# Optimization experiments

Measured on AMD Instinct MI355X. Metric: run time of the kernel, lower is better.

## Reference

```python
import jax, jax.numpy as jnp
import numpy as np

B, T, C, L = 512, 512, 96, 64   # batch, time steps, num classes (incl. blank), max label len
BLANK = C - 1                   # keras ctc_batch_cost uses last class as blank
EPS = 1e-7                      # epsilon added before log, as in ctc_batch_cost
NEG = -1e30                     # log-space -inf surrogate


def setup_inputs():
    key = jax.random.key(0)
    k1, k2, k3 = jax.random.split(key, 3)
    # y_pred is a softmax output: positive, rows sum to 1
    u = jax.random.uniform(k1, (B, T, C), dtype=jnp.float32, minval=0.1, maxval=1.0)
    y_pred = u / jnp.sum(u, axis=-1, keepdims=True)
    # labels in [0, BLANK), variable lengths, padded with -1 (as the layer expects)
    labels = jax.random.randint(k2, (B, L), 0, C - 1, dtype=jnp.int32)
    lens = jax.random.randint(k3, (B,), L // 2, L + 1, dtype=jnp.int32)
    y_true = jnp.where(jnp.arange(L)[None, :] < lens[:, None], labels, -1)
    return {"y_true": y_true, "y_pred": y_pred}


def _ctc_loss(y_true, y_pred):
    """Per-example CTC negative log-likelihood (forward DP in log space)."""
    y_true = y_true.astype(jnp.int32)
    lbl_len = jnp.sum((y_true != -1).astype(jnp.int32), axis=-1)          # (B,)
    labels = jnp.where(y_true != -1, y_true, 0)                            # (B,L)

    S = 2 * L + 1
    # extended label: blank, l0, blank, l1, ..., blank
    ext = jnp.full((B, S), BLANK, dtype=jnp.int32).at[:, 1::2].set(labels)  # (B,S)
    ext_m2 = jnp.pad(ext[:, :-2], ((0, 0), (2, 0)), constant_values=BLANK)
    can_skip = (ext != BLANK) & (ext != ext_m2)                             # (B,S)

    lp = jnp.log(y_pred.astype(jnp.float32) + EPS)   # (B,T,C) log-probs
    lp_t = jnp.swapaxes(lp, 0, 1)                    # (T,B,C) for scan over time

    emit0 = jnp.take_along_axis(lp_t[0], ext, axis=1)                       # (B,S)
    alpha0 = (jnp.full((B, S), NEG, dtype=jnp.float32)
              .at[:, 0].set(emit0[:, 0])
              .at[:, 1].set(emit0[:, 1]))

    def step(alpha, lpt):
        a1 = jnp.pad(alpha[:, :-1], ((0, 0), (1, 0)), constant_values=NEG)
        a2 = jnp.pad(alpha[:, :-2], ((0, 0), (2, 0)), constant_values=NEG)
        a2 = jnp.where(can_skip, a2, NEG)
        m = jnp.maximum(alpha, jnp.maximum(a1, a2))
        lse = m + jnp.log(jnp.exp(alpha - m) + jnp.exp(a1 - m) + jnp.exp(a2 - m))
        alpha_new = lse + jnp.take_along_axis(lpt, ext, axis=1)
        return alpha_new, None

    alphaT, _ = jax.lax.scan(step, alpha0, lp_t[1:])

    # total log-prob ends at last blank (s=2*len) or last label (s=2*len-1)
    i_blank = (2 * lbl_len)[:, None]
    i_label = jnp.maximum(2 * lbl_len - 1, 0)[:, None]
    a_b = jnp.take_along_axis(alphaT, i_blank, axis=1)[:, 0]
    a_l = jnp.take_along_axis(alphaT, i_label, axis=1)[:, 0]
    return -jnp.logaddexp(a_b, a_l)                                         # (B,)


def reference(y_true, y_pred):
    # layer adds tf.reduce_mean(ctc_batch_cost(...)) as the model loss
    return jnp.mean(_ctc_loss(y_true, y_pred))
```

## Files before the change

### kernel.cpp

```cpp
#include <hip/hip_runtime.h>


#define B_ 512
#define T_ 512
#define C_ 96
#define L_ 64
#define BLANK_ 95
#define EPSF 1e-7f
#define LN2F 0.69314718055994530942f

template <int CTRL>
__device__ __forceinline__ float dpp_mov(float x) {
    return __int_as_float(
        __builtin_amdgcn_update_dpp(0, __float_as_int(x), CTRL, 0xF, 0xF, true));
}

__device__ __forceinline__ float wave_max(float m) {
    m = fmaxf(m, dpp_mov<0x111>(m));
    m = fmaxf(m, dpp_mov<0x112>(m));
    m = fmaxf(m, dpp_mov<0x114>(m));
    m = fmaxf(m, dpp_mov<0x118>(m));
    m = fmaxf(m, dpp_mov<0x142>(m));
    m = fmaxf(m, dpp_mov<0x143>(m));
    return __int_as_float(__builtin_amdgcn_readlane(__float_as_int(m), 63));
}

__launch_bounds__(64, 1)
__global__ void ctc_loss_kernel(const int* __restrict__ y_true,
                                const float* __restrict__ y_pred,
                                float* __restrict__ out) {
    const int b = blockIdx.x;
    const int lane = threadIdx.x;

    const int yv = y_true[b * L_ + lane];
    const unsigned long long act = __ballot(yv != -1);
    const int len = __popcll(act);
    const int lab = (yv == -1) ? 0 : yv;
    const int lab_prev = __shfl_up(lab, 1);
    const bool cs = (lane == 0) ? true : (lab != lab_prev);

    const float* rowp = y_pred + (size_t)b * T_ * C_;
    const float* plp = rowp + lab;
    const float* pbp = rowp + BLANK_;

    constexpr int U = 8;
    constexpr int NCH = T_ / U;
    float bl[3][U], bb[3][U];
#pragma unroll
    for (int d = 0; d < 3; ++d)
#pragma unroll
        for (int k = 0; k < U; ++k) {
            bl[d][k] = plp[(d * U + k) * C_];
            bb[d][k] = pbp[(d * U + k) * C_];
        }

    float a_even, a_odd, a128;
    int accum = 0;
    {
        const float pb0 = bb[0][0] + EPSF;
        const float pl0 = bl[0][0] + EPSF;
        a_even = (lane == 0) ? pb0 : 0.0f;
        a_odd  = (lane == 0) ? pl0 : 0.0f;
        a128 = 0.0f;
    }

    auto step = [&](float rl, float rb) {
        const float pbv = rb + EPSF;
        const float plv = rl + EPSF;
        const float po = dpp_mov<0x138>(a_odd);
        const float pos = cs ? po : 0.0f;
        const float ne = (a_even + po) * pbv;
        const float no = (a_odd + a_even + pos) * plv;
        a128 = (a128 + a_odd) * pbv;
        a_even = ne;
        a_odd = no;
    };

    auto renorm = [&]() {
        const float mv = wave_max(fmaxf(fmaxf(a_even, a_odd), a128));
        const int e = ((__float_as_int(mv) >> 23) & 0xFF) - 126;
        const int k = 96 - e;
        a_even = ldexpf(a_even, k);
        a_odd  = ldexpf(a_odd, k);
        a128   = ldexpf(a128, k);
        accum -= k;
    };

    auto prefetch = [&](float* dl, float* db, int t0) {
#pragma unroll
        for (int k = 0; k < U; ++k) {
            dl[k] = plp[(t0 + k) * C_];
            db[k] = pbp[(t0 + k) * C_];
        }
    };

#pragma unroll
    for (int k = 1; k < U; ++k) step(bl[0][k], bb[0][k]);
    renorm();
    prefetch(bl[0], bb[0], 3 * U);

    for (int g = 0; g < 21; ++g) {
        const int cbase = 1 + g * 3;
#pragma unroll
        for (int sub = 0; sub < 3; ++sub) {
            const int slot = (sub + 1) % 3;
#pragma unroll
            for (int k = 0; k < U; ++k) step(bl[slot][k], bb[slot][k]);
            renorm();
            const int pc = cbase + sub + 3;
            if (pc < NCH) prefetch(bl[slot], bb[slot], pc * U);
        }
    }

    const float al = __shfl(a_odd, len - 1);
    const float ab = (len < L_) ? __shfl(a_even, len)
                                : __shfl(a128, 63);
    if (lane == 0) {
        const float loss = -LN2F * (log2f(ab + al) + (float)accum);
        atomicAdd(out, loss * (1.0f / B_));
    }
}

extern "C" void kernel_launch(void* const* d_in, const int* in_sizes, int n_in,
                              void* d_out, int out_size, void* d_ws, size_t ws_size,
                              hipStream_t stream) {
    const int* y_true = (const int*)d_in[0];
    const float* y_pred = (const float*)d_in[1];
    float* out = (float*)d_out;
    hipMemsetAsync(out, 0, sizeof(float), stream);
    ctc_loss_kernel<<<B_, 64, 0, stream>>>(y_true, y_pred, out);
}
```

Baseline: 155.6 us.

## Deepen prefetch pipeline to eight chunks and fuse step arithmetic with FMAs

The register prefetch ring grows from three to eight chunks of eight timesteps, so global loads for a chunk are issued about 64 steps before they are used. The aim is to hide memory latency better in this one-wave-per-block kernel. The recurrence step is rewritten with FMAs and precomputed masked label probabilities to shorten the dependent arithmetic chain. Alpha starts pre-scaled by 2^96 with a matching accumulator offset. The deeper ring raises register pressure, which is acceptable at one wave of occupancy but could spill if the compiler cannot fully unroll the ring indices.

```diff
diff --git a/kernel.cpp b/kernel.cpp
--- a/kernel.cpp
+++ b/kernel.cpp
@@ -44,10 +44,11 @@
     const float* pbp = rowp + BLANK_;
 
     constexpr int U = 8;
+    constexpr int D = 8;
     constexpr int NCH = T_ / U;
-    float bl[3][U], bb[3][U];
+    float bl[D][U], bb[D][U];
 #pragma unroll
-    for (int d = 0; d < 3; ++d)
+    for (int d = 0; d < D; ++d)
 #pragma unroll
         for (int k = 0; k < U; ++k) {
             bl[d][k] = plp[(d * U + k) * C_];
@@ -55,35 +56,36 @@
         }
 
     float a_even, a_odd, a128;
-    int accum = 0;
-    {
-        const float pb0 = bb[0][0] + EPSF;
-        const float pl0 = bl[0][0] + EPSF;
-        a_even = (lane == 0) ? pb0 : 0.0f;
-        a_odd  = (lane == 0) ? pl0 : 0.0f;
-        a128 = 0.0f;
-    }
+    int accum = -96;
+    a_even = (lane == 0) ? ldexpf(bb[0][0] + EPSF, 96) : 0.0f;
+    a_odd  = (lane == 0) ? ldexpf(bl[0][0] + EPSF, 96) : 0.0f;
+    a128 = 0.0f;
 
-    auto step = [&](float rl, float rb) {
-        const float pbv = rb + EPSF;
-        const float plv = rl + EPSF;
-        const float po = dpp_mov<0x138>(a_odd);
-        const float pos = cs ? po : 0.0f;
-        const float ne = (a_even + po) * pbv;
-        const float no = (a_odd + a_even + pos) * plv;
-        a128 = (a128 + a_odd) * pbv;
-        a_even = ne;
-        a_odd = no;
-    };
-
-    auto renorm = [&]() {
+    auto chunk_exec = [&](const float* cl, const float* cb, int kstart) {
+        float pl[U], pb[U], mpl[U];
+#pragma unroll
+        for (int k = 0; k < U; ++k) {
+            pl[k] = cl[k] + EPSF;
+            pb[k] = cb[k] + EPSF;
+            mpl[k] = cs ? pl[k] : 0.0f;
+        }
+#pragma unroll
+        for (int k = 0; k < U; ++k) {
+            if (k < kstart) continue;
+            const float po = dpp_mov<0x138>(a_odd);
+            const float ne = fmaf(po, pb[k], a_even * pb[k]);
+            const float no = fmaf(po, mpl[k], (a_odd + a_even) * pl[k]);
+            a128 = fmaf(a_odd, pb[k], a128 * pb[k]);
+            a_even = ne;
+            a_odd = no;
+        }
         const float mv = wave_max(fmaxf(fmaxf(a_even, a_odd), a128));
         const int e = ((__float_as_int(mv) >> 23) & 0xFF) - 126;
-        const int k = 96 - e;
-        a_even = ldexpf(a_even, k);
-        a_odd  = ldexpf(a_odd, k);
-        a128   = ldexpf(a128, k);
-        accum -= k;
+        const int kk = 96 - e;
+        a_even = ldexpf(a_even, kk);
+        a_odd  = ldexpf(a_odd, kk);
+        a128   = ldexpf(a128, kk);
+        accum -= kk;
     };
 
     auto prefetch = [&](float* dl, float* db, int t0) {
@@ -95,20 +97,17 @@
     };
 
 #pragma unroll
-    for (int k = 1; k < U; ++k) step(bl[0][k], bb[0][k]);
-    renorm();
-    prefetch(bl[0], bb[0], 3 * U);
+    for (int sub = 0; sub < D; ++sub) {
+        chunk_exec(bl[sub], bb[sub], (sub == 0) ? 1 : 0);
+        prefetch(bl[sub], bb[sub], (sub + D) * U);
+    }
 
-    for (int g = 0; g < 21; ++g) {
-        const int cbase = 1 + g * 3;
+    for (int g = 1; g < NCH / D; ++g) {
 #pragma unroll
-        for (int sub = 0; sub < 3; ++sub) {
-            const int slot = (sub + 1) % 3;
-#pragma unroll
-            for (int k = 0; k < U; ++k) step(bl[slot][k], bb[slot][k]);
-            renorm();
-            const int pc = cbase + sub + 3;
-            if (pc < NCH) prefetch(bl[slot], bb[slot], pc * U);
+        for (int sub = 0; sub < D; ++sub) {
+            const int c = g * D + sub;
+            chunk_exec(bl[sub], bb[sub], 0);
+            if (c + D < NCH) prefetch(bl[sub], bb[sub], (c + D) * U);
         }
     }
 
```

New measurement: 156.9 us. Within noise of the previous version (+0.8%).
